# Kernel optimization log

Hardware: AMD Instinct MI355X
Metric: run time of the kernel (lower is better)

Reference implementation:

```python
import jax, jax.numpy as jnp
import numpy as np

N, E = 20000, 160000
D_NODE_IN, D_EDGE_IN = 256, 64
D = 128          # node/edge feature dim
H = 256          # edge hidden dim
T = 17           # number of keypoint types
EDGE_STEPS, NODE_STEPS = 2, 1


def _w(k, shape):
    return jax.random.normal(k, shape, dtype=jnp.float32) / np.sqrt(shape[-2] if len(shape) > 1 else shape[-1]).astype(np.float32)


def setup_inputs() -> dict:
    key = jax.random.key(0)
    ks = iter(jax.random.split(key, 40))
    inp = {
        'x': jax.random.normal(next(ks), (N, D_NODE_IN), dtype=jnp.float32),
        'edge_attr': jax.random.normal(next(ks), (E, D_EDGE_IN), dtype=jnp.float32),
        'edge_index': jax.random.randint(next(ks), (2, E), 0, N),
        'node_types': jax.random.randint(next(ks), (N,), 0, T),
        # type-routed node embedding: 17 stacked 2-layer MLPs 256->128->128
        'ne_w1': _w(next(ks), (T, D_NODE_IN, D)), 'ne_b1': jnp.zeros((T, D)),
        'ne_w2': _w(next(ks), (T, D, D)),         'ne_b2': jnp.zeros((T, D)),
        # edge embedding 64->128->128
        'ee_w1': _w(next(ks), (D_EDGE_IN, D)), 'ee_b1': jnp.zeros((D,)),
        'ee_w2': _w(next(ks), (D, D)),         'ee_b2': jnp.zeros((D,)),
        # MPLayer edge MLP: [x_i, x_j, e] with skip -> (2*2D + 2D)=768 -> 256 -> 128
        'me_w1': _w(next(ks), (4 * D + 2 * D, H)), 'me_b1': jnp.zeros((H,)),
        'me_w2': _w(next(ks), (H, D)),             'me_b2': jnp.zeros((D,)),
        # MPLayer node update: [x(skip 2D), agg(D)] -> 128
        'mn_w1': _w(next(ks), (2 * D + D, D)), 'mn_b1': jnp.zeros((D,)),
        # classifiers
        'ec_w1': _w(next(ks), (D, D)), 'ec_b1': jnp.zeros((D,)),
        'ec_w2': _w(next(ks), (D, 1)), 'ec_b2': jnp.zeros((1,)),
        'nc_w1': _w(next(ks), (D, D)), 'nc_b1': jnp.zeros((D,)),
        'nc_w2': _w(next(ks), (D, 1)), 'nc_b2': jnp.zeros((1,)),
        'cc_w1': _w(next(ks), (D, D)), 'cc_b1': jnp.zeros((D,)),
        'cc_w2': _w(next(ks), (D, T)), 'cc_b2': jnp.zeros((T,)),
    }
    return inp


def _mlp2(x, w1, b1, w2, b2):
    return jax.nn.relu(x @ w1 + b1) @ w2 + b2


def reference(x, edge_attr, edge_index, node_types,
              ne_w1, ne_b1, ne_w2, ne_b2,
              ee_w1, ee_b1, ee_w2, ee_b2,
              me_w1, me_b1, me_w2, me_b2,
              mn_w1, mn_b1,
              ec_w1, ec_b1, ec_w2, ec_b2,
              nc_w1, nc_b1, nc_w2, nc_b2,
              cc_w1, cc_b1, cc_w2, cc_b2):
    n = x.shape[0]
    # NodeMlpType: run all 17 MLPs, select by node type (same math as masked dispatch)
    h = jax.nn.relu(jnp.einsum('nd,tdk->tnk', x, ne_w1) + ne_b1[:, None, :])   # [T,N,D]
    o = jnp.einsum('tnk,tkm->tnm', h, ne_w2) + ne_b2[:, None, :]               # [T,N,D]
    nf0 = o[node_types, jnp.arange(n)]                                          # [N,D]
    ef0 = _mlp2(edge_attr, ee_w1, ee_b1, ee_w2, ee_b2)                          # [E,D]

    src, dst = edge_index[0], edge_index[1]

    def mp_step(nf, ef):
        nf_c = jnp.concatenate([nf0, nf], axis=1)                               # skip concat [N,2D]
        ef_c = jnp.concatenate([ef0, ef], axis=1)                               # [E,2D]
        m = jnp.concatenate([nf_c[dst], nf_c[src], ef_c], axis=1)               # [E,6D]
        e_new = _mlp2(m, me_w1, me_b1, me_w2, me_b2)                            # [E,D]
        agg = jax.ops.segment_sum(e_new, dst, num_segments=n)                   # aggr='add'
        nf_new = jnp.concatenate([nf_c, agg], axis=1) @ mn_w1 + mn_b1           # [N,D]
        return nf_new, e_new

    nf, ef = nf0, ef0
    for _ in range(EDGE_STEPS):
        nf, ef = mp_step(nf, ef)
    pred_edge = _mlp2(ef, ec_w1, ec_b1, ec_w2, ec_b2).squeeze(-1)               # [E]
    for _ in range(NODE_STEPS):
        nf, ef = mp_step(nf, ef)
    pred_node = _mlp2(nf, nc_w1, nc_b1, nc_w2, nc_b2).squeeze(-1)               # [N]
    pred_class = _mlp2(nf, cc_w1, cc_b1, cc_w2, cc_b2)                          # [N,T]
    return (pred_edge, pred_node, pred_class, nf, ef)
```

## Files before the change

kernel.cpp:

```cpp
#include <hip/hip_runtime.h>
#include <hip/hip_bf16.h>

#define N_NODES 20000
#define N_EDGES 160000
#define DIN_NODE 256
#define DIN_EDGE 64
#define DF 128
#define HH 256
#define TT 17
#define NE_PAD_SLOTS 20544

typedef __attribute__((ext_vector_type(8))) short short8v;
typedef __attribute__((ext_vector_type(4))) float f32x4;

__device__ __forceinline__ unsigned short f2bf(float f) {
  unsigned int u = __builtin_bit_cast(unsigned int, f);
  u += 0x7FFFu + ((u >> 16) & 1u);
  return (unsigned short)(u >> 16);
}

__device__ __forceinline__ float bf2f(unsigned short u) {
  return __builtin_bit_cast(float, (unsigned int)u << 16);
}

__device__ __forceinline__ short8v pack8(float4 a, float4 b) {
  short8v o;
  o[0] = (short)f2bf(a.x); o[1] = (short)f2bf(a.y);
  o[2] = (short)f2bf(a.z); o[3] = (short)f2bf(a.w);
  o[4] = (short)f2bf(b.x); o[5] = (short)f2bf(b.y);
  o[6] = (short)f2bf(b.z); o[7] = (short)f2bf(b.w);
  return o;
}

__global__ __launch_bounds__(256) void k_pack_w(
    const float* __restrict__ w, unsigned short* __restrict__ out,
    int Kdim, int Ndim, int batch) {
  const int tile = blockIdx.x * 4 + (threadIdx.x >> 6);
  const int l = threadIdx.x & 63;
  const int ntTiles = Ndim >> 4;
  const int tilesPer = (Kdim >> 5) * ntTiles;
  if (tile >= tilesPer * batch) return;
  const int bt = tile / tilesPer;
  const int rr = tile - bt * tilesPer;
  const int kt = rr / ntTiles, nt = rr % ntTiles;
  const float* wb = w + (size_t)bt * Kdim * Ndim;
  const int col = (nt << 4) + (l & 15);
  const int k0 = (kt << 5) + ((l >> 4) << 3);
  unsigned short* o = out + (((size_t)tile << 6) + l) * 8;
#pragma unroll
  for (int j = 0; j < 8; ++j) o[j] = f2bf(wb[(size_t)(k0 + j) * Ndim + col]);
}

__global__ void k_count(const int* __restrict__ types, int* __restrict__ cnt) {
  const int n = blockIdx.x * 256 + threadIdx.x;
  if (n < N_NODES) atomicAdd(&cnt[types[n]], 1);
}
__global__ void k_prefix(const int* __restrict__ cnt, int* __restrict__ poff,
                         int* __restrict__ woff) {
  if (threadIdx.x == 0) {
    int cur = 0;
    for (int t = 0; t < TT; ++t) {
      poff[t] = cur; woff[t] = cur;
      cur += (cnt[t] + 31) & ~31;
    }
  }
}
__global__ void k_scatter(const int* __restrict__ types, int* __restrict__ woff,
                          int* __restrict__ bucket) {
  const int n = blockIdx.x * 256 + threadIdx.x;
  if (n < N_NODES) {
    const int pos = atomicAdd(&woff[types[n]], 1);
    bucket[pos] = n;
  }
}

__global__ void k_deg(const int* __restrict__ dstv, int* __restrict__ deg) {
  const int e = blockIdx.x * 256 + threadIdx.x;
  if (e < N_EDGES) atomicAdd(&deg[dstv[e]], 1);
}
__global__ __launch_bounds__(256) void k_scan(const int* __restrict__ deg,
                                              int* __restrict__ rs,
                                              int* __restrict__ wo) {
  __shared__ int partial[256];
  const int t = threadIdx.x;
  const int base = t * 80;
  int s = 0;
  for (int j = 0; j < 80; ++j) {
    const int n = base + j;
    if (n < N_NODES) s += deg[n];
  }
  partial[t] = s;
  __syncthreads();
  for (int off = 1; off < 256; off <<= 1) {
    const int v = (t >= off) ? partial[t - off] : 0;
    __syncthreads();
    partial[t] += v;
    __syncthreads();
  }
  int run = (t > 0) ? partial[t - 1] : 0;
  for (int j = 0; j < 80; ++j) {
    const int n = base + j;
    if (n < N_NODES) {
      rs[n] = run; wo[n] = run;
      run += deg[n];
    }
  }
  if (t == 255) rs[N_NODES] = run;
}
__global__ void k_elist(const int* __restrict__ dstv, int* __restrict__ wo,
                        int* __restrict__ elist) {
  const int e = blockIdx.x * 256 + threadIdx.x;
  if (e < N_EDGES) {
    const int pos = atomicAdd(&wo[dstv[e]], 1);
    elist[pos] = e;
  }
}

__global__ __launch_bounds__(256) void k_node_embed_mfma(
    const float* __restrict__ x, const int* __restrict__ bucket,
    const int* __restrict__ types,
    const unsigned short* __restrict__ wp1, const float* __restrict__ b1,
    const unsigned short* __restrict__ wp2, const float* __restrict__ b2,
    unsigned short* __restrict__ nf0b) {
  __shared__ __align__(16) unsigned char A[32 * 512];
  __shared__ __align__(16) unsigned char Hb[32 * 256];
  __shared__ int sn[32];
  const int t = threadIdx.x;
  const int r0 = blockIdx.x * 32;
  if (t < 32) sn[t] = bucket[r0 + t];
  __syncthreads();
  if (sn[0] < 0) return;
  const int ty = types[sn[0]];

#pragma unroll
  for (int j = 0; j < 4; ++j) {
    const int q = j * 256 + t;
    const int i = q >> 5, c = q & 31;
    const int nd = sn[i];
    short8v o;
    if (nd >= 0) {
      const float* xr = x + (size_t)nd * DIN_NODE + c * 8;
      o = pack8(*reinterpret_cast<const float4*>(xr),
                *reinterpret_cast<const float4*>(xr + 4));
    } else {
#pragma unroll
      for (int k = 0; k < 8; ++k) o[k] = 0;
    }
    *reinterpret_cast<short8v*>(A + ((i * 512 + c * 16) ^ ((i & 7) << 4))) = o;
  }
  __syncthreads();

  const int w = t >> 6, l = t & 63, lr = l & 15, lg = l >> 4;
  const int sw = (lr & 7) << 4;
  const int row0 = lr, row1 = 16 + lr;

  f32x4 acc[2][2];
#pragma unroll
  for (int mt = 0; mt < 2; ++mt)
#pragma unroll
    for (int q = 0; q < 2; ++q)
#pragma unroll
      for (int r = 0; r < 4; ++r) acc[mt][q][r] = 0.f;

#pragma unroll
  for (int kt = 0; kt < 8; ++kt) {
    const short8v a0 = *reinterpret_cast<const short8v*>(
        A + ((row0 * 512 + kt * 64 + lg * 16) ^ sw));
    const short8v a1 = *reinterpret_cast<const short8v*>(
        A + ((row1 * 512 + kt * 64 + lg * 16) ^ sw));
#pragma unroll
    for (int q = 0; q < 2; ++q) {
      const short8v bq = *reinterpret_cast<const short8v*>(
          wp1 + (((size_t)(ty * 64 + kt * 8 + 2 * w + q) * 64 + l) << 3));
      acc[0][q] = __builtin_amdgcn_mfma_f32_16x16x32_bf16(a0, bq, acc[0][q], 0, 0, 0);
      acc[1][q] = __builtin_amdgcn_mfma_f32_16x16x32_bf16(a1, bq, acc[1][q], 0, 0, 0);
    }
  }
#pragma unroll
  for (int q = 0; q < 2; ++q) {
    const int col = (2 * w + q) * 16 + lr;
    const float bias = b1[ty * DF + col];
#pragma unroll
    for (int mt = 0; mt < 2; ++mt)
#pragma unroll
      for (int r = 0; r < 4; ++r) {
        const int row = mt * 16 + lg * 4 + r;
        *reinterpret_cast<unsigned short*>(
            Hb + ((row * 256 + col * 2) ^ ((row & 7) << 4))) =
            f2bf(fmaxf(acc[mt][q][r] + bias, 0.f));
      }
  }
  __syncthreads();

  f32x4 acc2[2][2];
#pragma unroll
  for (int mt = 0; mt < 2; ++mt)
#pragma unroll
    for (int q = 0; q < 2; ++q)
#pragma unroll
      for (int r = 0; r < 4; ++r) acc2[mt][q][r] = 0.f;
#pragma unroll
  for (int kt = 0; kt < 4; ++kt) {
    const short8v a0 = *reinterpret_cast<const short8v*>(
        Hb + ((row0 * 256 + kt * 64 + lg * 16) ^ sw));
    const short8v a1 = *reinterpret_cast<const short8v*>(
        Hb + ((row1 * 256 + kt * 64 + lg * 16) ^ sw));
#pragma unroll
    for (int q = 0; q < 2; ++q) {
      const short8v bq = *reinterpret_cast<const short8v*>(
          wp2 + (((size_t)(ty * 32 + kt * 8 + 2 * w + q) * 64 + l) << 3));
      acc2[0][q] = __builtin_amdgcn_mfma_f32_16x16x32_bf16(a0, bq, acc2[0][q], 0, 0, 0);
      acc2[1][q] = __builtin_amdgcn_mfma_f32_16x16x32_bf16(a1, bq, acc2[1][q], 0, 0, 0);
    }
  }
#pragma unroll
  for (int q = 0; q < 2; ++q) {
    const int col = (2 * w + q) * 16 + lr;
    const float bias = b2[ty * DF + col];
#pragma unroll
    for (int mt = 0; mt < 2; ++mt)
#pragma unroll
      for (int r = 0; r < 4; ++r) {
        const int row = mt * 16 + lg * 4 + r;
        const int nd = sn[row];
        if (nd >= 0)
          nf0b[(size_t)nd * DF + col] = f2bf(acc2[mt][q][r] + bias);
      }
  }
}

__global__ __launch_bounds__(256) void k_edge_embed_mfma(
    const float* __restrict__ ea,
    const unsigned short* __restrict__ wp1, const float* __restrict__ b1,
    const unsigned short* __restrict__ wp2, const float* __restrict__ b2,
    unsigned short* __restrict__ ef0b) {
  __shared__ __align__(16) unsigned char A[32 * 128];
  __shared__ __align__(16) unsigned char Hb[32 * 256];
  const int t = threadIdx.x;
  const int e0 = blockIdx.x * 32;
  {
    const int i = t >> 3, c = t & 7;
    const float* xr = ea + (size_t)(e0 + i) * DIN_EDGE + c * 8;
    const short8v o = pack8(*reinterpret_cast<const float4*>(xr),
                            *reinterpret_cast<const float4*>(xr + 4));
    *reinterpret_cast<short8v*>(A + ((i * 128 + c * 16) ^ ((i & 7) << 4))) = o;
  }
  __syncthreads();

  const int w = t >> 6, l = t & 63, lr = l & 15, lg = l >> 4;
  const int sw = (lr & 7) << 4;
  const int row0 = lr, row1 = 16 + lr;

  f32x4 acc[2][2];
#pragma unroll
  for (int mt = 0; mt < 2; ++mt)
#pragma unroll
    for (int q = 0; q < 2; ++q)
#pragma unroll
      for (int r = 0; r < 4; ++r) acc[mt][q][r] = 0.f;
#pragma unroll
  for (int kt = 0; kt < 2; ++kt) {
    const short8v a0 = *reinterpret_cast<const short8v*>(
        A + ((row0 * 128 + kt * 64 + lg * 16) ^ sw));
    const short8v a1 = *reinterpret_cast<const short8v*>(
        A + ((row1 * 128 + kt * 64 + lg * 16) ^ sw));
#pragma unroll
    for (int q = 0; q < 2; ++q) {
      const short8v bq = *reinterpret_cast<const short8v*>(
          wp1 + (((size_t)(kt * 8 + 2 * w + q) * 64 + l) << 3));
      acc[0][q] = __builtin_amdgcn_mfma_f32_16x16x32_bf16(a0, bq, acc[0][q], 0, 0, 0);
      acc[1][q] = __builtin_amdgcn_mfma_f32_16x16x32_bf16(a1, bq, acc[1][q], 0, 0, 0);
    }
  }
#pragma unroll
  for (int q = 0; q < 2; ++q) {
    const int col = (2 * w + q) * 16 + lr;
    const float bias = b1[col];
#pragma unroll
    for (int mt = 0; mt < 2; ++mt)
#pragma unroll
      for (int r = 0; r < 4; ++r) {
        const int row = mt * 16 + lg * 4 + r;
        *reinterpret_cast<unsigned short*>(
            Hb + ((row * 256 + col * 2) ^ ((row & 7) << 4))) =
            f2bf(fmaxf(acc[mt][q][r] + bias, 0.f));
      }
  }
  __syncthreads();

  f32x4 acc2[2][2];
#pragma unroll
  for (int mt = 0; mt < 2; ++mt)
#pragma unroll
    for (int q = 0; q < 2; ++q)
#pragma unroll
      for (int r = 0; r < 4; ++r) acc2[mt][q][r] = 0.f;
#pragma unroll
  for (int kt = 0; kt < 4; ++kt) {
    const short8v a0 = *reinterpret_cast<const short8v*>(
        Hb + ((row0 * 256 + kt * 64 + lg * 16) ^ sw));
    const short8v a1 = *reinterpret_cast<const short8v*>(
        Hb + ((row1 * 256 + kt * 64 + lg * 16) ^ sw));
#pragma unroll
    for (int q = 0; q < 2; ++q) {
      const short8v bq = *reinterpret_cast<const short8v*>(
          wp2 + (((size_t)(kt * 8 + 2 * w + q) * 64 + l) << 3));
      acc2[0][q] = __builtin_amdgcn_mfma_f32_16x16x32_bf16(a0, bq, acc2[0][q], 0, 0, 0);
      acc2[1][q] = __builtin_amdgcn_mfma_f32_16x16x32_bf16(a1, bq, acc2[1][q], 0, 0, 0);
    }
  }
#pragma unroll
  for (int q = 0; q < 2; ++q) {
    const int col = (2 * w + q) * 16 + lr;
    const float bias = b2[col];
#pragma unroll
    for (int mt = 0; mt < 2; ++mt)
#pragma unroll
      for (int r = 0; r < 4; ++r) {
        const int row = mt * 16 + lg * 4 + r;
        ef0b[(size_t)(e0 + row) * DF + col] = f2bf(acc2[mt][q][r] + bias);
      }
  }
}

__global__ __launch_bounds__(256) void k_partial(
    const unsigned short* __restrict__ nf0b, const unsigned short* __restrict__ nfb,
    const unsigned short* __restrict__ wpd, const unsigned short* __restrict__ wps,
    unsigned short* __restrict__ PDo, unsigned short* __restrict__ PSo) {
  __shared__ __align__(16) unsigned char A[32 * 512];
  const int t = threadIdx.x;
  const int n0 = blockIdx.x * 32;
#pragma unroll
  for (int j = 0; j < 4; ++j) {
    const int q = j * 256 + t;
    const int i = q >> 5, c = q & 31;
    const unsigned short* bp = (c < 16)
        ? nf0b + (size_t)(n0 + i) * DF + c * 8
        : nfb + (size_t)(n0 + i) * DF + (c - 16) * 8;
    *reinterpret_cast<short8v*>(A + ((i * 512 + c * 16) ^ ((i & 7) << 4))) =
        *reinterpret_cast<const short8v*>(bp);
  }
  __syncthreads();

  const int w = t >> 6, l = t & 63, lr = l & 15, lg = l >> 4;
  const int swz = (lr & 7) << 4;
  const int r0o = lr * 512 + lg * 16, r1o = (16 + lr) * 512 + lg * 16;

  f32x4 aD[2][4], aS[2][4];
#pragma unroll
  for (int mt = 0; mt < 2; ++mt)
#pragma unroll
    for (int q = 0; q < 4; ++q)
#pragma unroll
      for (int r = 0; r < 4; ++r) { aD[mt][q][r] = 0.f; aS[mt][q][r] = 0.f; }

#pragma unroll
  for (int kt = 0; kt < 8; ++kt) {
    const short8v a0 = *reinterpret_cast<const short8v*>(A + ((r0o + kt * 64) ^ swz));
    const short8v a1 = *reinterpret_cast<const short8v*>(A + ((r1o + kt * 64) ^ swz));
#pragma unroll
    for (int q = 0; q < 4; ++q) {
      const size_t bi = (((size_t)(kt * 16 + 4 * w + q) * 64 + l) << 3);
      const short8v bD = *reinterpret_cast<const short8v*>(wpd + bi);
      const short8v bS = *reinterpret_cast<const short8v*>(wps + bi);
      aD[0][q] = __builtin_amdgcn_mfma_f32_16x16x32_bf16(a0, bD, aD[0][q], 0, 0, 0);
      aD[1][q] = __builtin_amdgcn_mfma_f32_16x16x32_bf16(a1, bD, aD[1][q], 0, 0, 0);
      aS[0][q] = __builtin_amdgcn_mfma_f32_16x16x32_bf16(a0, bS, aS[0][q], 0, 0, 0);
      aS[1][q] = __builtin_amdgcn_mfma_f32_16x16x32_bf16(a1, bS, aS[1][q], 0, 0, 0);
    }
  }
#pragma unroll
  for (int q = 0; q < 4; ++q) {
    const int col = (4 * w + q) * 16 + lr;
#pragma unroll
    for (int mt = 0; mt < 2; ++mt)
#pragma unroll
      for (int r = 0; r < 4; ++r) {
        const int row = mt * 16 + lg * 4 + r;
        PDo[(size_t)(n0 + row) * HH + col] = f2bf(aD[mt][q][r]);
        PSo[(size_t)(n0 + row) * HH + col] = f2bf(aS[mt][q][r]);
      }
  }
}

template <bool OUTF, bool HEAD>
__global__ __launch_bounds__(256) void k_edge_mlp_mfma(
    const unsigned short* __restrict__ ef0, const unsigned short* __restrict__ ef_in,
    void* __restrict__ ef_out,
    const int* __restrict__ srcv, const int* __restrict__ dstv,
    const unsigned short* __restrict__ wpe, const float* __restrict__ b1,
    const unsigned short* __restrict__ wp2, const float* __restrict__ b2,
    const unsigned short* __restrict__ PDi, const unsigned short* __restrict__ PSi,
    const unsigned short* __restrict__ wech, const float* __restrict__ hb1,
    const float* __restrict__ hw2, const float* __restrict__ hb2,
    float* __restrict__ out_pe) {
  __shared__ __align__(16) unsigned char A_lds[32 * 512];
  __shared__ __align__(16) unsigned char P_lds[32 * 512];
  __shared__ int sd[2][32];
  __shared__ float hpart[32][8];
  const int t = threadIdx.x;
  const int e0 = blockIdx.x * 32;
  if (t < 32) sd[0][t] = srcv[e0 + t];
  else if (t < 64) sd[1][t - 32] = dstv[e0 + t - 32];

#pragma unroll
  for (int j = 0; j < 4; ++j) {
    const int q = j * 256 + t;
    const int i = q >> 5, c = q & 31;
    const unsigned short* bp = (c < 16)
        ? ef0 + (size_t)(e0 + i) * DF + c * 8
        : ef_in + (size_t)(e0 + i) * DF + (c - 16) * 8;
    *reinterpret_cast<short8v*>(A_lds + ((i * 512 + c * 16) ^ ((i & 7) << 4))) =
        *reinterpret_cast<const short8v*>(bp);
  }
  __syncthreads();

#pragma unroll
  for (int j = 0; j < 4; ++j) {
    const int q = j * 256 + t;
    const int i = q >> 5, c = q & 31;
    const short8v pd = *reinterpret_cast<const short8v*>(
        PDi + (size_t)sd[1][i] * HH + c * 8);
    const short8v ps = *reinterpret_cast<const short8v*>(
        PSi + (size_t)sd[0][i] * HH + c * 8);
    short8v o;
#pragma unroll
    for (int k = 0; k < 8; ++k)
      o[k] = (short)f2bf(bf2f((unsigned short)pd[k]) + bf2f((unsigned short)ps[k]));
    *reinterpret_cast<short8v*>(P_lds + ((i * 512 + c * 16) ^ ((i & 7) << 4))) = o;
  }
  __syncthreads();

  const int w = t >> 6, l = t & 63, lr = l & 15, lg = l >> 4;
  const int swz = (lr & 7) << 4;

  f32x4 acc[2][4];
#pragma unroll
  for (int mt = 0; mt < 2; ++mt)
#pragma unroll
    for (int q = 0; q < 4; ++q) {
      const int col = (4 * w + q) * 16 + lr;
#pragma unroll
      for (int r = 0; r < 4; ++r) {
        const int row = mt * 16 + lg * 4 + r;
        const unsigned short u = *reinterpret_cast<const unsigned short*>(
            P_lds + ((row * 512 + col * 2) ^ ((row & 7) << 4)));
        acc[mt][q][r] = bf2f(u);
      }
    }

  const int r0o = lr * 512 + lg * 16;
  const int r1o = (16 + lr) * 512 + lg * 16;
  const unsigned short* wb1 = wpe + (((size_t)(4 * w) * 64 + l) << 3);

  short8v aR[3][2], bR[3][4];
#pragma unroll
  for (int s = 0; s < 2; ++s) {
    aR[s][0] = *reinterpret_cast<const short8v*>(A_lds + ((r0o + s * 64) ^ swz));
    aR[s][1] = *reinterpret_cast<const short8v*>(A_lds + ((r1o + s * 64) ^ swz));
#pragma unroll
    for (int q = 0; q < 4; ++q)
      bR[s][q] = *reinterpret_cast<const short8v*>(wb1 + (size_t)s * 8192 + q * 512);
  }
#pragma unroll
  for (int kt = 0; kt < 8; ++kt) {
    const int cur = kt % 3, pf = (kt + 2) % 3;
    if (kt < 6) {
      aR[pf][0] = *reinterpret_cast<const short8v*>(
          A_lds + ((r0o + (kt + 2) * 64) ^ swz));
      aR[pf][1] = *reinterpret_cast<const short8v*>(
          A_lds + ((r1o + (kt + 2) * 64) ^ swz));
#pragma unroll
      for (int q = 0; q < 4; ++q)
        bR[pf][q] = *reinterpret_cast<const short8v*>(
            wb1 + (size_t)(kt + 2) * 8192 + q * 512);
    }
#pragma unroll
    for (int q = 0; q < 4; ++q) {
      acc[0][q] = __builtin_amdgcn_mfma_f32_16x16x32_bf16(aR[cur][0], bR[cur][q],
                                                          acc[0][q], 0, 0, 0);
      acc[1][q] = __builtin_amdgcn_mfma_f32_16x16x32_bf16(aR[cur][1], bR[cur][q],
                                                          acc[1][q], 0, 0, 0);
    }
  }
  __syncthreads();

#pragma unroll
  for (int q = 0; q < 4; ++q) {
    const int col = (4 * w + q) * 16 + lr;
    const float bias = b1[col];
#pragma unroll
    for (int mt = 0; mt < 2; ++mt)
#pragma unroll
      for (int r = 0; r < 4; ++r) {
        const int row = mt * 16 + lg * 4 + r;
        *reinterpret_cast<unsigned short*>(
            P_lds + ((row * 512 + col * 2) ^ ((row & 7) << 4))) =
            f2bf(fmaxf(acc[mt][q][r] + bias, 0.f));
      }
  }
  __syncthreads();

  f32x4 acc2[2][2];
#pragma unroll
  for (int mt = 0; mt < 2; ++mt)
#pragma unroll
    for (int q = 0; q < 2; ++q)
#pragma unroll
      for (int r = 0; r < 4; ++r) acc2[mt][q][r] = 0.f;

  const int h0o = lr * 512 + lg * 16;
  const int h1o = (16 + lr) * 512 + lg * 16;
  const unsigned short* wb2 = wp2 + (((size_t)(2 * w) * 64 + l) << 3);

  short8v aS[3][2], bS[3][2];
#pragma unroll
  for (int s = 0; s < 2; ++s) {
    aS[s][0] = *reinterpret_cast<const short8v*>(P_lds + ((h0o + s * 64) ^ swz));
    aS[s][1] = *reinterpret_cast<const short8v*>(P_lds + ((h1o + s * 64) ^ swz));
#pragma unroll
    for (int q = 0; q < 2; ++q)
      bS[s][q] = *reinterpret_cast<const short8v*>(wb2 + (size_t)s * 4096 + q * 512);
  }
#pragma unroll
  for (int kt = 0; kt < 8; ++kt) {
    const int cur = kt % 3, pf = (kt + 2) % 3;
    if (kt < 6) {
      aS[pf][0] = *reinterpret_cast<const short8v*>(
          P_lds + ((h0o + (kt + 2) * 64) ^ swz));
      aS[pf][1] = *reinterpret_cast<const short8v*>(
          P_lds + ((h1o + (kt + 2) * 64) ^ swz));
#pragma unroll
      for (int q = 0; q < 2; ++q)
        bS[pf][q] = *reinterpret_cast<const short8v*>(
            wb2 + (size_t)(kt + 2) * 4096 + q * 512);
    }
#pragma unroll
    for (int q = 0; q < 2; ++q) {
      acc2[0][q] = __builtin_amdgcn_mfma_f32_16x16x32_bf16(aS[cur][0], bS[cur][q],
                                                           acc2[0][q], 0, 0, 0);
      acc2[1][q] = __builtin_amdgcn_mfma_f32_16x16x32_bf16(aS[cur][1], bS[cur][q],
                                                           acc2[1][q], 0, 0, 0);
    }
  }

#pragma unroll
  for (int q = 0; q < 2; ++q) {
    const int n = (2 * w + q) * 16 + lr;
    const float bias = b2[n];
#pragma unroll
    for (int mt = 0; mt < 2; ++mt)
#pragma unroll
      for (int r = 0; r < 4; ++r) {
        const int m = mt * 16 + lg * 4 + r;
        const float v = acc2[mt][q][r] + bias;
        if (OUTF)
          ((float*)ef_out)[(size_t)(e0 + m) * DF + n] = v;
        else
          ((unsigned short*)ef_out)[(size_t)(e0 + m) * DF + n] = f2bf(v);
      }
  }

  if constexpr (HEAD) {
    __syncthreads();
#pragma unroll
    for (int q = 0; q < 2; ++q) {
      const int n = (2 * w + q) * 16 + lr;
      const float bias = b2[n];
#pragma unroll
      for (int mt = 0; mt < 2; ++mt)
#pragma unroll
        for (int r = 0; r < 4; ++r) {
          const int m = mt * 16 + lg * 4 + r;
          *reinterpret_cast<unsigned short*>(
              P_lds + ((m * 256 + n * 2) ^ ((m & 7) << 4))) =
              f2bf(acc2[mt][q][r] + bias);
        }
    }
    __syncthreads();
    f32x4 ah[2][2];
#pragma unroll
    for (int mt = 0; mt < 2; ++mt)
#pragma unroll
      for (int q = 0; q < 2; ++q)
#pragma unroll
        for (int r = 0; r < 4; ++r) ah[mt][q][r] = 0.f;
#pragma unroll
    for (int kt = 0; kt < 4; ++kt) {
      const short8v a0 = *reinterpret_cast<const short8v*>(
          P_lds + ((lr * 256 + kt * 64 + lg * 16) ^ swz));
      const short8v a1 = *reinterpret_cast<const short8v*>(
          P_lds + (((16 + lr) * 256 + kt * 64 + lg * 16) ^ swz));
#pragma unroll
      for (int q = 0; q < 2; ++q) {
        const short8v bq = *reinterpret_cast<const short8v*>(
            wech + (((size_t)(kt * 8 + 2 * w + q) * 64 + l) << 3));
        ah[0][q] = __builtin_amdgcn_mfma_f32_16x16x32_bf16(a0, bq, ah[0][q], 0, 0, 0);
        ah[1][q] = __builtin_amdgcn_mfma_f32_16x16x32_bf16(a1, bq, ah[1][q], 0, 0, 0);
      }
    }
#pragma unroll
    for (int q = 0; q < 2; ++q) {
      const int col = (2 * w + q) * 16 + lr;
      const float bias = hb1[col];
#pragma unroll
      for (int mt = 0; mt < 2; ++mt)
#pragma unroll
        for (int r = 0; r < 4; ++r) {
          const int row = mt * 16 + lg * 4 + r;
          *reinterpret_cast<unsigned short*>(A_lds + row * 256 + col * 2) =
              f2bf(fmaxf(ah[mt][q][r] + bias, 0.f));
        }
    }
    __syncthreads();
    {
      const int rr = t >> 3, kc = t & 7;
      float s = 0.f;
#pragma unroll
      for (int u = 0; u < 16; ++u)
        s = fmaf(bf2f(*reinterpret_cast<const unsigned short*>(
                     A_lds + rr * 256 + (kc * 16 + u) * 2)),
                 hw2[kc * 16 + u], s);
      hpart[rr][kc] = s;
    }
    __syncthreads();
    if (t < 32) {
      float s = hb2[0];
#pragma unroll
      for (int k = 0; k < 8; ++k) s += hpart[t][k];
      out_pe[e0 + t] = s;
    }
  }
}

template <bool OUTF, bool PART>
__global__ __launch_bounds__(256) void k_node_update_mfma(
    const unsigned short* __restrict__ nf0, const unsigned short* __restrict__ nfb,
    const void* __restrict__ efrows,
    const int* __restrict__ rs, const int* __restrict__ elist,
    void* __restrict__ outp,
    const unsigned short* __restrict__ wp, const float* __restrict__ b,
    const unsigned short* __restrict__ wpd, const unsigned short* __restrict__ wps,
    unsigned short* __restrict__ PDo, unsigned short* __restrict__ PSo) {
  __shared__ __align__(16) unsigned char A[32 * 768];
  const int t = threadIdx.x;
  const int n0 = blockIdx.x * 32;
#pragma unroll
  for (int j = 0; j < 4; ++j) {
    const int q = j * 256 + t;
    const int i = q >> 5, c = q & 31;
    const unsigned short* bp = (c < 16)
        ? nf0 + (size_t)(n0 + i) * DF + c * 8
        : nfb + (size_t)(n0 + i) * DF + (c - 16) * 8;
    *reinterpret_cast<short8v*>(A + ((i * 768 + c * 16) ^ ((i & 7) << 4))) =
        *reinterpret_cast<const short8v*>(bp);
  }
  {
    const int i = t >> 3, sub = t & 7;
    const int n = n0 + i;
    const int kb = rs[n], ke = rs[n + 1];
    float av[16];
#pragma unroll
    for (int u = 0; u < 16; ++u) av[u] = 0.f;
    for (int k = kb; k < ke; ++k) {
      const int e = elist[k];
      if (OUTF) {
        const float* er = (const float*)efrows + (size_t)e * DF + sub * 16;
#pragma unroll
        for (int u4 = 0; u4 < 4; ++u4) {
          const float4 f = *reinterpret_cast<const float4*>(er + u4 * 4);
          av[u4 * 4 + 0] += f.x; av[u4 * 4 + 1] += f.y;
          av[u4 * 4 + 2] += f.z; av[u4 * 4 + 3] += f.w;
        }
      } else {
        const unsigned short* er =
            (const unsigned short*)efrows + (size_t)e * DF + sub * 16;
        const short8v v0 = *reinterpret_cast<const short8v*>(er);
        const short8v v1 = *reinterpret_cast<const short8v*>(er + 8);
#pragma unroll
        for (int u = 0; u < 8; ++u) {
          av[u] += bf2f((unsigned short)v0[u]);
          av[8 + u] += bf2f((unsigned short)v1[u]);
        }
      }
    }
    short8v o0, o1;
#pragma unroll
    for (int u = 0; u < 8; ++u) {
      o0[u] = (short)f2bf(av[u]);
      o1[u] = (short)f2bf(av[8 + u]);
    }
    const int c0 = 32 + sub * 2;
    *reinterpret_cast<short8v*>(A + ((i * 768 + c0 * 16) ^ ((i & 7) << 4))) = o0;
    *reinterpret_cast<short8v*>(A + ((i * 768 + (c0 + 1) * 16) ^ ((i & 7) << 4))) = o1;
  }
  __syncthreads();

  const int w = t >> 6, l = t & 63, lr = l & 15, lg = l >> 4;
  const int sw = (lr & 7) << 4;
  const int row0 = lr, row1 = 16 + lr;

  f32x4 acc[2][2];
#pragma unroll
  for (int mt = 0; mt < 2; ++mt)
#pragma unroll
    for (int q = 0; q < 2; ++q)
#pragma unroll
      for (int r = 0; r < 4; ++r) acc[mt][q][r] = 0.f;
#pragma unroll
  for (int kt = 0; kt < 12; ++kt) {
    const short8v a0 = *reinterpret_cast<const short8v*>(
        A + ((row0 * 768 + kt * 64 + lg * 16) ^ sw));
    const short8v a1 = *reinterpret_cast<const short8v*>(
        A + ((row1 * 768 + kt * 64 + lg * 16) ^ sw));
#pragma unroll
    for (int q = 0; q < 2; ++q) {
      const short8v bq = *reinterpret_cast<const short8v*>(
          wp + (((size_t)(kt * 8 + 2 * w + q) * 64 + l) << 3));
      acc[0][q] = __builtin_amdgcn_mfma_f32_16x16x32_bf16(a0, bq, acc[0][q], 0, 0, 0);
      acc[1][q] = __builtin_amdgcn_mfma_f32_16x16x32_bf16(a1, bq, acc[1][q], 0, 0, 0);
    }
  }
#pragma unroll
  for (int q = 0; q < 2; ++q) {
    const int col = (2 * w + q) * 16 + lr;
    const float bias = b[col];
#pragma unroll
    for (int mt = 0; mt < 2; ++mt)
#pragma unroll
      for (int r = 0; r < 4; ++r) {
        const int row = mt * 16 + lg * 4 + r;
        const float v = acc[mt][q][r] + bias;
        if (OUTF)
          ((float*)outp)[(size_t)(n0 + row) * DF + col] = v;
        else
          ((unsigned short*)outp)[(size_t)(n0 + row) * DF + col] = f2bf(v);
      }
  }

  if constexpr (PART) {
    __syncthreads();
#pragma unroll
    for (int q = 0; q < 2; ++q) {
      const int col = (2 * w + q) * 16 + lr;
      const float bias = b[col];
#pragma unroll
      for (int mt = 0; mt < 2; ++mt)
#pragma unroll
        for (int r = 0; r < 4; ++r) {
          const int row = mt * 16 + lg * 4 + r;
          *reinterpret_cast<unsigned short*>(
              A + ((row * 768 + 256 + col * 2) ^ ((row & 7) << 4))) =
              f2bf(acc[mt][q][r] + bias);
        }
    }
    __syncthreads();
    f32x4 aD[2][4], aSv[2][4];
#pragma unroll
    for (int mt = 0; mt < 2; ++mt)
#pragma unroll
      for (int q = 0; q < 4; ++q)
#pragma unroll
        for (int r = 0; r < 4; ++r) { aD[mt][q][r] = 0.f; aSv[mt][q][r] = 0.f; }
    const int r0p = lr * 768 + lg * 16, r1p = (16 + lr) * 768 + lg * 16;
#pragma unroll
    for (int kt = 0; kt < 8; ++kt) {
      const short8v a0 = *reinterpret_cast<const short8v*>(A + ((r0p + kt * 64) ^ sw));
      const short8v a1 = *reinterpret_cast<const short8v*>(A + ((r1p + kt * 64) ^ sw));
#pragma unroll
      for (int q = 0; q < 4; ++q) {
        const size_t bi = (((size_t)(kt * 16 + 4 * w + q) * 64 + l) << 3);
        const short8v bD = *reinterpret_cast<const short8v*>(wpd + bi);
        const short8v bSv = *reinterpret_cast<const short8v*>(wps + bi);
        aD[0][q] = __builtin_amdgcn_mfma_f32_16x16x32_bf16(a0, bD, aD[0][q], 0, 0, 0);
        aD[1][q] = __builtin_amdgcn_mfma_f32_16x16x32_bf16(a1, bD, aD[1][q], 0, 0, 0);
        aSv[0][q] = __builtin_amdgcn_mfma_f32_16x16x32_bf16(a0, bSv, aSv[0][q], 0, 0, 0);
        aSv[1][q] = __builtin_amdgcn_mfma_f32_16x16x32_bf16(a1, bSv, aSv[1][q], 0, 0, 0);
      }
    }
#pragma unroll
    for (int q = 0; q < 4; ++q) {
      const int col = (4 * w + q) * 16 + lr;
#pragma unroll
      for (int mt = 0; mt < 2; ++mt)
#pragma unroll
        for (int r = 0; r < 4; ++r) {
          const int row = mt * 16 + lg * 4 + r;
          PDo[(size_t)(n0 + row) * HH + col] = f2bf(aD[mt][q][r]);
          PSo[(size_t)(n0 + row) * HH + col] = f2bf(aSv[mt][q][r]);
        }
    }
  }
}

template <bool INBF>
__global__ __launch_bounds__(256) void k_cls_scalar_mfma(
    const void* __restrict__ feat, const unsigned short* __restrict__ wp,
    const float* __restrict__ b1, const float* __restrict__ w2,
    const float* __restrict__ b2, float* __restrict__ out) {
  __shared__ __align__(16) unsigned char A[32 * 256];
  __shared__ float hid[32][136];
  __shared__ float w2s[DF];
  __shared__ float part[32][8];
  const int t = threadIdx.x;
  const int r0 = blockIdx.x * 32;
  if (t < DF) w2s[t] = w2[t];
#pragma unroll
  for (int j = 0; j < 2; ++j) {
    const int q = j * 256 + t;
    const int i = q >> 4, c = q & 15;
    short8v o;
    if (INBF) {
      o = *reinterpret_cast<const short8v*>(
          (const unsigned short*)feat + (size_t)(r0 + i) * DF + c * 8);
    } else {
      const float* fr = (const float*)feat + (size_t)(r0 + i) * DF + c * 8;
      o = pack8(*reinterpret_cast<const float4*>(fr),
                *reinterpret_cast<const float4*>(fr + 4));
    }
    *reinterpret_cast<short8v*>(A + ((i * 256 + c * 16) ^ ((i & 7) << 4))) = o;
  }
  __syncthreads();

  const int w = t >> 6, l = t & 63, lr = l & 15, lg = l >> 4;
  const int sw = (lr & 7) << 4;
  const int row0 = lr, row1 = 16 + lr;
  f32x4 acc[2][2];
#pragma unroll
  for (int mt = 0; mt < 2; ++mt)
#pragma unroll
    for (int q = 0; q < 2; ++q)
#pragma unroll
      for (int r = 0; r < 4; ++r) acc[mt][q][r] = 0.f;
#pragma unroll
  for (int kt = 0; kt < 4; ++kt) {
    const short8v a0 = *reinterpret_cast<const short8v*>(
        A + ((row0 * 256 + kt * 64 + lg * 16) ^ sw));
    const short8v a1 = *reinterpret_cast<const short8v*>(
        A + ((row1 * 256 + kt * 64 + lg * 16) ^ sw));
#pragma unroll
    for (int q = 0; q < 2; ++q) {
      const short8v bq = *reinterpret_cast<const short8v*>(
          wp + (((size_t)(kt * 8 + 2 * w + q) * 64 + l) << 3));
      acc[0][q] = __builtin_amdgcn_mfma_f32_16x16x32_bf16(a0, bq, acc[0][q], 0, 0, 0);
      acc[1][q] = __builtin_amdgcn_mfma_f32_16x16x32_bf16(a1, bq, acc[1][q], 0, 0, 0);
    }
  }
#pragma unroll
  for (int q = 0; q < 2; ++q) {
    const int col = (2 * w + q) * 16 + lr;
    const float bias = b1[col];
#pragma unroll
    for (int mt = 0; mt < 2; ++mt)
#pragma unroll
      for (int r = 0; r < 4; ++r) {
        const int row = mt * 16 + lg * 4 + r;
        hid[row][col] = fmaxf(acc[mt][q][r] + bias, 0.f);
      }
  }
  __syncthreads();
  {
    const int r = t >> 3, kc = t & 7;
    float s = 0.f;
#pragma unroll
    for (int u = 0; u < 16; ++u) s = fmaf(hid[r][kc * 16 + u], w2s[kc * 16 + u], s);
    part[r][kc] = s;
  }
  __syncthreads();
  if (t < 32) {
    float s = b2[0];
#pragma unroll
    for (int k = 0; k < 8; ++k) s += part[t][k];
    out[r0 + t] = s;
  }
}

__global__ __launch_bounds__(256) void k_cls_class_mfma(
    const float* __restrict__ feat, const unsigned short* __restrict__ wp,
    const float* __restrict__ b1, const float* __restrict__ w2,
    const float* __restrict__ b2, float* __restrict__ out) {
  __shared__ __align__(16) unsigned char A[32 * 256];
  __shared__ float hid[32][136];
  __shared__ float w2s[DF * TT];
  const int t = threadIdx.x;
  const int r0 = blockIdx.x * 32;
  for (int j = t; j < DF * TT; j += 256) w2s[j] = w2[j];
#pragma unroll
  for (int j = 0; j < 2; ++j) {
    const int q = j * 256 + t;
    const int i = q >> 4, c = q & 15;
    const float* fr = feat + (size_t)(r0 + i) * DF + c * 8;
    const short8v o = pack8(*reinterpret_cast<const float4*>(fr),
                            *reinterpret_cast<const float4*>(fr + 4));
    *reinterpret_cast<short8v*>(A + ((i * 256 + c * 16) ^ ((i & 7) << 4))) = o;
  }
  __syncthreads();

  const int w = t >> 6, l = t & 63, lr = l & 15, lg = l >> 4;
  const int sw = (lr & 7) << 4;
  const int row0 = lr, row1 = 16 + lr;
  f32x4 acc[2][2];
#pragma unroll
  for (int mt = 0; mt < 2; ++mt)
#pragma unroll
    for (int q = 0; q < 2; ++q)
#pragma unroll
      for (int r = 0; r < 4; ++r) acc[mt][q][r] = 0.f;
#pragma unroll
  for (int kt = 0; kt < 4; ++kt) {
    const short8v a0 = *reinterpret_cast<const short8v*>(
        A + ((row0 * 256 + kt * 64 + lg * 16) ^ sw));
    const short8v a1 = *reinterpret_cast<const short8v*>(
        A + ((row1 * 256 + kt * 64 + lg * 16) ^ sw));
#pragma unroll
    for (int q = 0; q < 2; ++q) {
      const short8v bq = *reinterpret_cast<const short8v*>(
          wp + (((size_t)(kt * 8 + 2 * w + q) * 64 + l) << 3));
      acc[0][q] = __builtin_amdgcn_mfma_f32_16x16x32_bf16(a0, bq, acc[0][q], 0, 0, 0);
      acc[1][q] = __builtin_amdgcn_mfma_f32_16x16x32_bf16(a1, bq, acc[1][q], 0, 0, 0);
    }
  }
#pragma unroll
  for (int q = 0; q < 2; ++q) {
    const int col = (2 * w + q) * 16 + lr;
    const float bias = b1[col];
#pragma unroll
    for (int mt = 0; mt < 2; ++mt)
#pragma unroll
      for (int r = 0; r < 4; ++r) {
        const int row = mt * 16 + lg * 4 + r;
        hid[row][col] = fmaxf(acc[mt][q][r] + bias, 0.f);
      }
  }
  __syncthreads();
  for (int o = t; o < 32 * TT; o += 256) {
    const int r = o / TT, c = o - TT * r;
    float s = b2[c];
    for (int k = 0; k < DF; ++k) s = fmaf(hid[r][k], w2s[k * TT + c], s);
    out[(size_t)(r0 + r) * TT + c] = s;
  }
}

extern "C" void kernel_launch(void* const* d_in, const int* in_sizes, int n_in,
                              void* d_out, int out_size, void* d_ws,
                              size_t ws_size, hipStream_t stream) {
  (void)in_sizes; (void)n_in; (void)out_size; (void)ws_size;
  const float* x         = (const float*)d_in[0];
  const float* edge_attr = (const float*)d_in[1];
  const int*   edge_idx  = (const int*)d_in[2];
  const int*   node_ty   = (const int*)d_in[3];
  const float* ne_w1 = (const float*)d_in[4];
  const float* ne_b1 = (const float*)d_in[5];
  const float* ne_w2 = (const float*)d_in[6];
  const float* ne_b2 = (const float*)d_in[7];
  const float* ee_w1 = (const float*)d_in[8];
  const float* ee_b1 = (const float*)d_in[9];
  const float* ee_w2 = (const float*)d_in[10];
  const float* ee_b2 = (const float*)d_in[11];
  const float* me_w1 = (const float*)d_in[12];
  const float* me_b1 = (const float*)d_in[13];
  const float* me_w2 = (const float*)d_in[14];
  const float* me_b2 = (const float*)d_in[15];
  const float* mn_w1 = (const float*)d_in[16];
  const float* mn_b1 = (const float*)d_in[17];
  const float* ec_w1 = (const float*)d_in[18];
  const float* ec_b1 = (const float*)d_in[19];
  const float* ec_w2 = (const float*)d_in[20];
  const float* ec_b2 = (const float*)d_in[21];
  const float* nc_w1 = (const float*)d_in[22];
  const float* nc_b1 = (const float*)d_in[23];
  const float* nc_w2 = (const float*)d_in[24];
  const float* nc_b2 = (const float*)d_in[25];
  const float* cc_w1 = (const float*)d_in[26];
  const float* cc_b1 = (const float*)d_in[27];
  const float* cc_w2 = (const float*)d_in[28];
  const float* cc_b2 = (const float*)d_in[29];

  const int* srcv = edge_idx;
  const int* dstv = edge_idx + N_EDGES;

  unsigned short* nf0b = (unsigned short*)d_ws;
  unsigned short* nf1b = nf0b + (size_t)N_NODES * DF;
  unsigned short* ef0b = nf1b + (size_t)N_NODES * DF;
  unsigned short* ef1b = ef0b + (size_t)N_EDGES * DF;
  unsigned short* wmpD = ef1b + (size_t)N_EDGES * DF;
  unsigned short* wmpS = wmpD + 256 * 256;
  unsigned short* wmeE = wmpS + 256 * 256;
  unsigned short* wme2 = wmeE + 256 * 256;
  unsigned short* wmn  = wme2 + 256 * 128;
  unsigned short* wne1 = wmn + 384 * 128;
  unsigned short* wne2 = wne1 + (size_t)TT * 256 * 128;
  unsigned short* wee1 = wne2 + (size_t)TT * 128 * 128;
  unsigned short* wee2 = wee1 + 64 * 128;
  unsigned short* wec  = wee2 + 128 * 128;
  unsigned short* wnc  = wec + 128 * 128;
  unsigned short* wcc  = wnc + 128 * 128;
  unsigned short* PD   = wcc + 128 * 128;
  unsigned short* PS   = PD + (size_t)N_NODES * HH;
  int* cnt    = (int*)(PS + (size_t)N_NODES * HH);
  int* poff   = cnt + 32;
  int* woff   = poff + 32;
  int* bucket = woff + 32;
  int* deg    = bucket + NE_PAD_SLOTS;
  int* rs     = deg + N_NODES;
  int* wo     = rs + N_NODES + 1;
  int* elist  = wo + N_NODES;

  float* out_pe = (float*)d_out;
  float* out_pn = out_pe + N_EDGES;
  float* out_pc = out_pn + N_NODES;
  float* out_nf = out_pc + (size_t)N_NODES * TT;
  float* out_ef = out_nf + (size_t)N_NODES * DF;

  k_pack_w<<<32, 256, 0, stream>>>(me_w1, wmpD, 256, 256, 1);
  k_pack_w<<<32, 256, 0, stream>>>(me_w1 + 256 * 256, wmpS, 256, 256, 1);
  k_pack_w<<<32, 256, 0, stream>>>(me_w1 + 512 * 256, wmeE, 256, 256, 1);
  k_pack_w<<<16, 256, 0, stream>>>(me_w2, wme2, 256, 128, 1);
  k_pack_w<<<24, 256, 0, stream>>>(mn_w1, wmn, 384, 128, 1);
  k_pack_w<<<272, 256, 0, stream>>>(ne_w1, wne1, 256, 128, TT);
  k_pack_w<<<136, 256, 0, stream>>>(ne_w2, wne2, 128, 128, TT);
  k_pack_w<<<4, 256, 0, stream>>>(ee_w1, wee1, 64, 128, 1);
  k_pack_w<<<8, 256, 0, stream>>>(ee_w2, wee2, 128, 128, 1);
  k_pack_w<<<8, 256, 0, stream>>>(ec_w1, wec, 128, 128, 1);
  k_pack_w<<<8, 256, 0, stream>>>(nc_w1, wnc, 128, 128, 1);
  k_pack_w<<<8, 256, 0, stream>>>(cc_w1, wcc, 128, 128, 1);

  hipMemsetAsync(cnt, 0, 32 * sizeof(int), stream);
  hipMemsetAsync(bucket, 0xFF, NE_PAD_SLOTS * sizeof(int), stream);
  k_count<<<(N_NODES + 255) / 256, 256, 0, stream>>>(node_ty, cnt);
  k_prefix<<<1, 64, 0, stream>>>(cnt, poff, woff);
  k_scatter<<<(N_NODES + 255) / 256, 256, 0, stream>>>(node_ty, woff, bucket);

  hipMemsetAsync(deg, 0, N_NODES * sizeof(int), stream);
  k_deg<<<(N_EDGES + 255) / 256, 256, 0, stream>>>(dstv, deg);
  k_scan<<<1, 256, 0, stream>>>(deg, rs, wo);
  k_elist<<<(N_EDGES + 255) / 256, 256, 0, stream>>>(dstv, wo, elist);

  k_node_embed_mfma<<<NE_PAD_SLOTS / 32, 256, 0, stream>>>(
      x, bucket, node_ty, wne1, ne_b1, wne2, ne_b2, nf0b);
  k_edge_embed_mfma<<<N_EDGES / 32, 256, 0, stream>>>(edge_attr, wee1, ee_b1,
                                                      wee2, ee_b2, ef0b);

  k_partial<<<N_NODES / 32, 256, 0, stream>>>(nf0b, nf0b, wmpD, wmpS, PD, PS);
  k_edge_mlp_mfma<false, false><<<N_EDGES / 32, 256, 0, stream>>>(
      ef0b, ef0b, (void*)ef1b, srcv, dstv, wmeE, me_b1, wme2, me_b2, PD, PS,
      nullptr, nullptr, nullptr, nullptr, nullptr);
  k_node_update_mfma<false, true><<<N_NODES / 32, 256, 0, stream>>>(
      nf0b, nf0b, (const void*)ef1b, rs, elist, (void*)nf1b, wmn, mn_b1,
      wmpD, wmpS, PD, PS);
  k_edge_mlp_mfma<false, true><<<N_EDGES / 32, 256, 0, stream>>>(
      ef0b, ef1b, (void*)ef1b, srcv, dstv, wmeE, me_b1, wme2, me_b2, PD, PS,
      wec, ec_b1, ec_w2, ec_b2, out_pe);
  k_node_update_mfma<false, true><<<N_NODES / 32, 256, 0, stream>>>(
      nf0b, nf1b, (const void*)ef1b, rs, elist, (void*)nf1b, wmn, mn_b1,
      wmpD, wmpS, PD, PS);
  k_edge_mlp_mfma<true, false><<<N_EDGES / 32, 256, 0, stream>>>(
      ef0b, ef1b, (void*)out_ef, srcv, dstv, wmeE, me_b1, wme2, me_b2, PD, PS,
      nullptr, nullptr, nullptr, nullptr, nullptr);
  k_node_update_mfma<true, false><<<N_NODES / 32, 256, 0, stream>>>(
      nf0b, nf1b, (const void*)out_ef, rs, elist, (void*)out_nf, wmn, mn_b1,
      wmpD, wmpS, PD, PS);

  k_cls_scalar_mfma<false><<<N_NODES / 32, 256, 0, stream>>>(
      (const void*)out_nf, wnc, nc_b1, nc_w2, nc_b2, out_pn);
  k_cls_class_mfma<<<N_NODES / 32, 256, 0, stream>>>(out_nf, wcc, cc_b1, cc_w2,
                                                     cc_b2, out_pc);
}
```

Baseline: 651.3 us.

## Store edge features in destination-sorted order for contiguous aggregation

Edge feature buffers are now kept in CSR (destination-sorted) order. The edge embedding scatters its rows to their permuted positions, and the edge MLP reads permuted src/dst index arrays. The node-update aggregation can then read contiguous rows instead of gathering through elist. Final outputs (edge predictions and fp32 edge features) are scattered back to the original edge order via elist. This adds a permutation kernel, extra index arrays and scattered output writes, and the last node update now sums bf16 rows instead of fp32 ones.

```diff
diff --git a/kernel.cpp b/kernel.cpp
--- a/kernel.cpp
+++ b/kernel.cpp
@@ -108,11 +108,23 @@
   if (t == 255) rs[N_NODES] = run;
 }
 __global__ void k_elist(const int* __restrict__ dstv, int* __restrict__ wo,
-                        int* __restrict__ elist) {
+                        int* __restrict__ elist, int* __restrict__ ipos) {
   const int e = blockIdx.x * 256 + threadIdx.x;
   if (e < N_EDGES) {
     const int pos = atomicAdd(&wo[dstv[e]], 1);
     elist[pos] = e;
+    ipos[e] = pos;
+  }
+}
+__global__ void k_perm_sd(const int* __restrict__ elist,
+                          const int* __restrict__ srcv,
+                          const int* __restrict__ dstv,
+                          int* __restrict__ srcp, int* __restrict__ dstp) {
+  const int p = blockIdx.x * 256 + threadIdx.x;
+  if (p < N_EDGES) {
+    const int e = elist[p];
+    srcp[p] = srcv[e];
+    dstp[p] = dstv[e];
   }
 }
 
@@ -230,14 +242,16 @@
 }
 
 __global__ __launch_bounds__(256) void k_edge_embed_mfma(
-    const float* __restrict__ ea,
+    const float* __restrict__ ea, const int* __restrict__ ipos,
     const unsigned short* __restrict__ wp1, const float* __restrict__ b1,
     const unsigned short* __restrict__ wp2, const float* __restrict__ b2,
-    unsigned short* __restrict__ ef0b) {
+    unsigned short* __restrict__ ef0p) {
   __shared__ __align__(16) unsigned char A[32 * 128];
   __shared__ __align__(16) unsigned char Hb[32 * 256];
+  __shared__ int ip[32];
   const int t = threadIdx.x;
   const int e0 = blockIdx.x * 32;
+  if (t < 32) ip[t] = ipos[e0 + t];
   {
     const int i = t >> 3, c = t & 7;
     const float* xr = ea + (size_t)(e0 + i) * DIN_EDGE + c * 8;
@@ -318,7 +332,7 @@
 #pragma unroll
       for (int r = 0; r < 4; ++r) {
         const int row = mt * 16 + lg * 4 + r;
-        ef0b[(size_t)(e0 + row) * DF + col] = f2bf(acc2[mt][q][r] + bias);
+        ef0p[(size_t)ip[row] * DF + col] = f2bf(acc2[mt][q][r] + bias);
       }
   }
 }
@@ -386,8 +400,9 @@
 template <bool OUTF, bool HEAD>
 __global__ __launch_bounds__(256) void k_edge_mlp_mfma(
     const unsigned short* __restrict__ ef0, const unsigned short* __restrict__ ef_in,
-    void* __restrict__ ef_out,
-    const int* __restrict__ srcv, const int* __restrict__ dstv,
+    unsigned short* __restrict__ ef_out, float* __restrict__ ef_outf,
+    const int* __restrict__ srcp, const int* __restrict__ dstp,
+    const int* __restrict__ elist,
     const unsigned short* __restrict__ wpe, const float* __restrict__ b1,
     const unsigned short* __restrict__ wp2, const float* __restrict__ b2,
     const unsigned short* __restrict__ PDi, const unsigned short* __restrict__ PSi,
@@ -397,11 +412,13 @@
   __shared__ __align__(16) unsigned char A_lds[32 * 512];
   __shared__ __align__(16) unsigned char P_lds[32 * 512];
   __shared__ int sd[2][32];
+  __shared__ int se[32];
   __shared__ float hpart[32][8];
   const int t = threadIdx.x;
   const int e0 = blockIdx.x * 32;
-  if (t < 32) sd[0][t] = srcv[e0 + t];
-  else if (t < 64) sd[1][t - 32] = dstv[e0 + t - 32];
+  if (t < 32) sd[0][t] = srcp[e0 + t];
+  else if (t < 64) sd[1][t - 32] = dstp[e0 + t - 32];
+  else if ((OUTF || HEAD) && t < 96) se[t - 64] = elist[e0 + t - 64];
 
 #pragma unroll
   for (int j = 0; j < 4; ++j) {
@@ -554,10 +571,9 @@
       for (int r = 0; r < 4; ++r) {
         const int m = mt * 16 + lg * 4 + r;
         const float v = acc2[mt][q][r] + bias;
+        ef_out[(size_t)(e0 + m) * DF + n] = f2bf(v);
         if (OUTF)
-          ((float*)ef_out)[(size_t)(e0 + m) * DF + n] = v;
-        else
-          ((unsigned short*)ef_out)[(size_t)(e0 + m) * DF + n] = f2bf(v);
+          ef_outf[(size_t)se[m] * DF + n] = v;
       }
   }
 
@@ -628,7 +644,7 @@
       float s = hb2[0];
 #pragma unroll
       for (int k = 0; k < 8; ++k) s += hpart[t][k];
-      out_pe[e0 + t] = s;
+      out_pe[se[t]] = s;
     }
   }
 }
@@ -636,9 +652,8 @@
 template <bool OUTF, bool PART>
 __global__ __launch_bounds__(256) void k_node_update_mfma(
     const unsigned short* __restrict__ nf0, const unsigned short* __restrict__ nfb,
-    const void* __restrict__ efrows,
-    const int* __restrict__ rs, const int* __restrict__ elist,
-    void* __restrict__ outp,
+    const unsigned short* __restrict__ efp,
+    const int* __restrict__ rs, void* __restrict__ outp,
     const unsigned short* __restrict__ wp, const float* __restrict__ b,
     const unsigned short* __restrict__ wpd, const unsigned short* __restrict__ wps,
     unsigned short* __restrict__ PDo, unsigned short* __restrict__ PSo) {
@@ -663,25 +678,13 @@
 #pragma unroll
     for (int u = 0; u < 16; ++u) av[u] = 0.f;
     for (int k = kb; k < ke; ++k) {
-      const int e = elist[k];
-      if (OUTF) {
-        const float* er = (const float*)efrows + (size_t)e * DF + sub * 16;
-#pragma unroll
-        for (int u4 = 0; u4 < 4; ++u4) {
-          const float4 f = *reinterpret_cast<const float4*>(er + u4 * 4);
-          av[u4 * 4 + 0] += f.x; av[u4 * 4 + 1] += f.y;
-          av[u4 * 4 + 2] += f.z; av[u4 * 4 + 3] += f.w;
-        }
-      } else {
-        const unsigned short* er =
-            (const unsigned short*)efrows + (size_t)e * DF + sub * 16;
-        const short8v v0 = *reinterpret_cast<const short8v*>(er);
-        const short8v v1 = *reinterpret_cast<const short8v*>(er + 8);
-#pragma unroll
-        for (int u = 0; u < 8; ++u) {
-          av[u] += bf2f((unsigned short)v0[u]);
-          av[8 + u] += bf2f((unsigned short)v1[u]);
-        }
+      const unsigned short* er = efp + (size_t)k * DF + sub * 16;
+      const short8v v0 = *reinterpret_cast<const short8v*>(er);
+      const short8v v1 = *reinterpret_cast<const short8v*>(er + 8);
+#pragma unroll
+      for (int u = 0; u < 8; ++u) {
+        av[u] += bf2f((unsigned short)v0[u]);
+        av[8 + u] += bf2f((unsigned short)v1[u]);
       }
     }
     short8v o0, o1;
@@ -981,9 +984,9 @@
 
   unsigned short* nf0b = (unsigned short*)d_ws;
   unsigned short* nf1b = nf0b + (size_t)N_NODES * DF;
-  unsigned short* ef0b = nf1b + (size_t)N_NODES * DF;
-  unsigned short* ef1b = ef0b + (size_t)N_EDGES * DF;
-  unsigned short* wmpD = ef1b + (size_t)N_EDGES * DF;
+  unsigned short* ef0p = nf1b + (size_t)N_NODES * DF;
+  unsigned short* ef1p = ef0p + (size_t)N_EDGES * DF;
+  unsigned short* wmpD = ef1p + (size_t)N_EDGES * DF;
   unsigned short* wmpS = wmpD + 256 * 256;
   unsigned short* wmeE = wmpS + 256 * 256;
   unsigned short* wme2 = wmeE + 256 * 256;
@@ -1005,6 +1008,9 @@
   int* rs     = deg + N_NODES;
   int* wo     = rs + N_NODES + 1;
   int* elist  = wo + N_NODES;
+  int* ipos   = elist + N_EDGES;
+  int* srcp   = ipos + N_EDGES;
+  int* dstp   = srcp + N_EDGES;
 
   float* out_pe = (float*)d_out;
   float* out_pn = out_pe + N_EDGES;
@@ -1034,32 +1040,31 @@
   hipMemsetAsync(deg, 0, N_NODES * sizeof(int), stream);
   k_deg<<<(N_EDGES + 255) / 256, 256, 0, stream>>>(dstv, deg);
   k_scan<<<1, 256, 0, stream>>>(deg, rs, wo);
-  k_elist<<<(N_EDGES + 255) / 256, 256, 0, stream>>>(dstv, wo, elist);
+  k_elist<<<(N_EDGES + 255) / 256, 256, 0, stream>>>(dstv, wo, elist, ipos);
+  k_perm_sd<<<(N_EDGES + 255) / 256, 256, 0, stream>>>(elist, srcv, dstv, srcp,
+                                                       dstp);
 
   k_node_embed_mfma<<<NE_PAD_SLOTS / 32, 256, 0, stream>>>(
       x, bucket, node_ty, wne1, ne_b1, wne2, ne_b2, nf0b);
-  k_edge_embed_mfma<<<N_EDGES / 32, 256, 0, stream>>>(edge_attr, wee1, ee_b1,
-                                                      wee2, ee_b2, ef0b);
+  k_edge_embed_mfma<<<N_EDGES / 32, 256, 0, stream>>>(edge_attr, ipos, wee1,
+                                                      ee_b1, wee2, ee_b2, ef0p);
 
   k_partial<<<N_NODES / 32, 256, 0, stream>>>(nf0b, nf0b, wmpD, wmpS, PD, PS);
   k_edge_mlp_mfma<false, false><<<N_EDGES / 32, 256, 0, stream>>>(
-      ef0b, ef0b, (void*)ef1b, srcv, dstv, wmeE, me_b1, wme2, me_b2, PD, PS,
-      nullptr, nullptr, nullptr, nullptr, nullptr);
+      ef0p, ef0p, ef1p, nullptr, srcp, dstp, elist, wmeE, me_b1, wme2, me_b2,
+      PD, PS, nullptr, nullptr, nullptr, nullptr, nullptr);
   k_node_update_mfma<false, true><<<N_NODES / 32, 256, 0, stream>>>(
-      nf0b, nf0b, (const void*)ef1b, rs, elist, (void*)nf1b, wmn, mn_b1,
-      wmpD, wmpS, PD, PS);
+      nf0b, nf0b, ef1p, rs, (void*)nf1b, wmn, mn_b1, wmpD, wmpS, PD, PS);
   k_edge_mlp_mfma<false, true><<<N_EDGES / 32, 256, 0, stream>>>(
-      ef0b, ef1b, (void*)ef1b, srcv, dstv, wmeE, me_b1, wme2, me_b2, PD, PS,
-      wec, ec_b1, ec_w2, ec_b2, out_pe);
+      ef0p, ef1p, ef1p, nullptr, srcp, dstp, elist, wmeE, me_b1, wme2, me_b2,
+      PD, PS, wec, ec_b1, ec_w2, ec_b2, out_pe);
   k_node_update_mfma<false, true><<<N_NODES / 32, 256, 0, stream>>>(
-      nf0b, nf1b, (const void*)ef1b, rs, elist, (void*)nf1b, wmn, mn_b1,
-      wmpD, wmpS, PD, PS);
+      nf0b, nf1b, ef1p, rs, (void*)nf1b, wmn, mn_b1, wmpD, wmpS, PD, PS);
   k_edge_mlp_mfma<true, false><<<N_EDGES / 32, 256, 0, stream>>>(
-      ef0b, ef1b, (void*)out_ef, srcv, dstv, wmeE, me_b1, wme2, me_b2, PD, PS,
-      nullptr, nullptr, nullptr, nullptr, nullptr);
+      ef0p, ef1p, ef1p, out_ef, srcp, dstp, elist, wmeE, me_b1, wme2, me_b2,
+      PD, PS, nullptr, nullptr, nullptr, nullptr, nullptr);
   k_node_update_mfma<true, false><<<N_NODES / 32, 256, 0, stream>>>(
-      nf0b, nf1b, (const void*)out_ef, rs, elist, (void*)out_nf, wmn, mn_b1,
-      wmpD, wmpS, PD, PS);
+      nf0b, nf1b, ef1p, rs, (void*)out_nf, wmn, mn_b1, wmpD, wmpS, PD, PS);
 
   k_cls_scalar_mfma<false><<<N_NODES / 32, 256, 0, stream>>>(
       (const void*)out_nf, wnc, nc_b1, nc_w2, nc_b2, out_pn);
```

New measurement: 628.3 us. -3.5%, faster.
